# Optimization experiments

Hardware: AMD Instinct MI355X
Metric: run time of the kernel (lower is better)

## Reference

```python
import jax, jax.numpy as jnp
import numpy as np

N_NODES = 100000
N_EDGES = 1600000
N_FEAT = 165
HIDDEN = 128
N_CLASSES = 2
NEG_SLOPE = 0.2


def setup_inputs() -> dict:
    key = jax.random.key(0)
    ks = jax.random.split(key, 16)
    s = 0.05
    return {
        'x': jax.random.normal(ks[0], (N_NODES, N_FEAT), jnp.float32),
        'edge_src': jax.random.randint(ks[1], (N_EDGES,), 0, N_NODES, jnp.int32),
        'edge_dst': jax.random.randint(ks[2], (N_EDGES,), 0, N_NODES, jnp.int32),
        'W1l': jax.random.normal(ks[3], (N_FEAT, HIDDEN), jnp.float32) * s,
        'b1l': jnp.zeros((HIDDEN,), jnp.float32),
        'W1r': jax.random.normal(ks[4], (N_FEAT, HIDDEN), jnp.float32) * s,
        'b1r': jnp.zeros((HIDDEN,), jnp.float32),
        'att1': jax.random.normal(ks[5], (HIDDEN,), jnp.float32) * s,
        'bias1': jnp.zeros((HIDDEN,), jnp.float32),
        'W2l': jax.random.normal(ks[6], (HIDDEN, N_CLASSES), jnp.float32) * s,
        'b2l': jnp.zeros((N_CLASSES,), jnp.float32),
        'W2r': jax.random.normal(ks[7], (HIDDEN, N_CLASSES), jnp.float32) * s,
        'b2r': jnp.zeros((N_CLASSES,), jnp.float32),
        'att2': jax.random.normal(ks[8], (N_CLASSES,), jnp.float32) * s,
        'bias2': jnp.zeros((N_CLASSES,), jnp.float32),
    }


def gatv2_conv(x, src, dst, Wl, bl, Wr, br, att, bias, n_nodes):
    # PyG GATv2Conv, heads=1: x_l for source/message, x_r for target
    xl = x @ Wl + bl            # [N, D_out]
    xr = x @ Wr + br            # [N, D_out]
    e = jax.nn.leaky_relu(xl[src] + xr[dst], NEG_SLOPE)  # [E, D_out]
    score = e @ att             # [E]
    # segment softmax over destination nodes (stable)
    m = jax.ops.segment_max(score, dst, num_segments=n_nodes)
    a = jnp.exp(score - m[dst])
    denom = jax.ops.segment_sum(a, dst, num_segments=n_nodes)
    alpha = a / denom[dst]      # [E]
    out = jax.ops.segment_sum(alpha[:, None] * xl[src], dst, num_segments=n_nodes)
    return out + bias


def reference(x, edge_src, edge_dst, W1l, b1l, W1r, b1r, att1, bias1,
              W2l, b2l, W2r, b2r, att2, bias2):
    n = x.shape[0]
    # GATv2Conv adds self loops by default; every node has >=1 incoming edge
    loops = jnp.arange(n, dtype=edge_src.dtype)
    src = jnp.concatenate([edge_src, loops])
    dst = jnp.concatenate([edge_dst, loops])
    h = gatv2_conv(x, src, dst, W1l, b1l, W1r, b1r, att1, bias1, n)
    h = jax.nn.relu(h)
    # F.dropout with training=False is identity (eval mode)
    out = gatv2_conv(h, src, dst, W2l, b2l, W2r, b2r, att2, bias2, n)
    return out
```

## Files before the change

kernel.cpp:

```cpp
#include <hip/hip_runtime.h>
#include <hip/hip_bf16.h>

#define N_NODES 100000
#define NPAD 100032
#define N_EDGES 1600000
#define ETOT (N_EDGES + N_NODES)
#define NFEAT 165
#define KP 192
#define HID 128
#define NCLS 2
#define NEG 0.2f

#define NBUCK 391
#define CHUNK 16384
#define NCHUNK 104
#define GS_BLOCKS 2048

typedef short bf16x8 __attribute__((ext_vector_type(8)));
typedef float f32x4 __attribute__((ext_vector_type(4)));

#define OFF_FLAG 0
#define OFF_W 16
#define WO_ATT1 42496
#define WO_BIAS1 42624
#define WO_W2L 42752
#define WO_B2L 43008
#define WO_W2R 43010
#define WO_B2R 43266
#define WO_ATT2 43268
#define WO_BIAS2 43270

#define OFF_XB   43392
#define OFF_W2A  OFF_XB
#define OFF_WT   (OFF_XB + NPAD * KP / 2)
#define OFF_BCAT (OFF_WT + 256 * KP / 2)
#define OFF_XLB  (OFF_BCAT + 256)
#define OFF_XRB  (OFF_XLB + NPAD * HID / 2)
#define OFF_PAIRS (OFF_XRB + NPAD * HID / 2)
#define OFF_CSR  (OFF_PAIRS + 2 * ETOT)
#define OFF_ROWPTR (OFF_CSR + ETOT)
#define OFF_S    (OFF_ROWPTR + N_NODES + 8)
#define OFF_XL2  (OFF_S + NBUCK * NCHUNK + 8)
#define OFF_XR2  (OFF_XL2 + N_NODES * NCLS)
#define OFF_H    (OFF_XR2 + N_NODES * NCLS)
#define OFF_DL   (OFF_H + N_NODES * HID)
#define OFF_DR   (OFF_DL + NPAD)

__device__ __forceinline__ float bload16(unsigned short u) {
    return __uint_as_float(((unsigned)u) << 16);
}

__device__ __forceinline__ float lrelu(float v) {
    return fmaf(0.4f, fabsf(v), 0.6f * v);
}

__device__ __forceinline__ void unpack8(uint4 q, float* f) {
    f[0] = __uint_as_float(q.x << 16); f[1] = __uint_as_float(q.x & 0xffff0000u);
    f[2] = __uint_as_float(q.y << 16); f[3] = __uint_as_float(q.y & 0xffff0000u);
    f[4] = __uint_as_float(q.z << 16); f[5] = __uint_as_float(q.z & 0xffff0000u);
    f[6] = __uint_as_float(q.w << 16); f[7] = __uint_as_float(q.w & 0xffff0000u);
}

__device__ __forceinline__ unsigned short f2b(float f) {
    __hip_bfloat16 b = __float2bfloat16(f);
    return *(unsigned short*)&b;
}

__device__ __forceinline__ unsigned pack2(float a, float b) {
    return (unsigned)f2b(a) | ((unsigned)f2b(b) << 16);
}

__device__ __forceinline__ unsigned detect_flag(const unsigned short* x16, int lane) {
    unsigned short hh = x16[lane];
    unsigned e = (hh >> 7) & 0xFF;
    bool pl = ((hh & 0x7FFF) == 0) || (e >= 100 && e <= 140);
    unsigned long long m = __ballot(pl);
    return (__popcll(m) >= 52) ? 1u : 0u;
}

#define PREP_WT 49152
#define PREP_BC (PREP_WT + 256)
#define PREP_TOT (PREP_BC + 776)
#define PREP_BLKS ((PREP_TOT + 255) / 256)
__global__ void __launch_bounds__(256) k_prep_hist(
        const int* __restrict__ edst, int* __restrict__ bh,
        const unsigned short* __restrict__ x16,
        const void* W1l, const void* b1l, const void* W1r, const void* b1r,
        const void* att1, const void* bias1, const void* W2l, const void* b2l,
        const void* W2r, const void* b2r, const void* att2, const void* bias2,
        unsigned* __restrict__ flagp, unsigned short* __restrict__ wt,
        float* __restrict__ bcat, float* __restrict__ wb,
        float* __restrict__ w2a) {
    __shared__ int hist[NBUCK];
    if (blockIdx.x < NCHUNK) {
        for (int i = threadIdx.x; i < NBUCK; i += 256) hist[i] = 0;
        __syncthreads();
        int base = blockIdx.x * CHUNK;
        for (int i = threadIdx.x; i < CHUNK; i += 256) {
            int e = base + i;
            if (e >= ETOT) break;
            int d = (e < N_EDGES) ? edst[e] : (e - N_EDGES);
            atomicAdd(&hist[d >> 8], 1);
        }
        __syncthreads();
        for (int b = threadIdx.x; b < NBUCK; b += 256)
            bh[b * NCHUNK + blockIdx.x] = hist[b];
        return;
    }
    int lane = threadIdx.x & 63;
    unsigned isbf = detect_flag(x16, lane);
    int i = (blockIdx.x - NCHUNK) * 256 + threadIdx.x;
    if (i == 0) *flagp = isbf;
    if (i >= PREP_TOT) return;
    if (i < PREP_WT) {
        int n = i / KP, k = i - n * KP;
        unsigned short v = 0;
        if (k < NFEAT) {
            const void* src = (n < HID) ? W1l : W1r;
            size_t off = (size_t)k * HID + (n & (HID - 1));
            v = isbf ? ((const unsigned short*)src)[off]
                     : f2b(((const float*)src)[off]);
        }
        wt[i] = v;
    } else if (i < PREP_BC) {
        int n = i - PREP_WT;
        const void* src = (n < HID) ? b1l : b1r;
        int off = n & (HID - 1);
        bcat[n] = isbf ? bload16(((const unsigned short*)src)[off])
                       : ((const float*)src)[off];
    } else {
        int j = i - PREP_BC;
        const void* src; int off; int dst;
        if      (j < 128) { src = att1;  off = j;       dst = WO_ATT1 + j; }
        else if (j < 256) { src = bias1; off = j - 128; dst = WO_BIAS1 + (j - 128); }
        else if (j < 512) { src = W2l;   off = j - 256; dst = WO_W2L + (j - 256); }
        else if (j < 514) { src = b2l;   off = j - 512; dst = WO_B2L + (j - 512); }
        else if (j < 770) { src = W2r;   off = j - 514; dst = WO_W2R + (j - 514); }
        else if (j < 772) { src = b2r;   off = j - 770; dst = WO_B2R + (j - 770); }
        else if (j < 774) { src = att2;  off = j - 772; dst = WO_ATT2 + (j - 772); }
        else              { src = bias2; off = j - 774; dst = WO_BIAS2 + (j - 774); }
        float val = isbf ? bload16(((const unsigned short*)src)[off])
                         : ((const float*)src)[off];
        wb[dst] = val;
        if (j >= 256 && j < 512) w2a[j - 256] = val;
        else if (j >= 514 && j < 770) w2a[256 + (j - 514)] = val;
    }
}

__global__ void __launch_bounds__(512) k_pa_scan(int* __restrict__ S,
                                                 int* __restrict__ rowptr) {
    __shared__ int lds[512];
    const int TOT4 = (NBUCK * NCHUNK) / 4;
    int t = threadIdx.x;
    int b4 = t * 20;
    uint4* S4 = (uint4*)S;
    int sum = 0;
    for (int k = 0; k < 20; k++) {
        int i = b4 + k;
        if (i < TOT4) {
            uint4 v = S4[i];
            sum += (int)(v.x + v.y + v.z + v.w);
        }
    }
    lds[t] = sum;
    __syncthreads();
    for (int off = 1; off < 512; off <<= 1) {
        int v = lds[t];
        if (t >= off) v += lds[t - off];
        __syncthreads();
        lds[t] = v;
        __syncthreads();
    }
    int carry = (t == 0) ? 0 : lds[t - 1];
    for (int k = 0; k < 20; k++) {
        int i = b4 + k;
        if (i < TOT4) {
            uint4 v = S4[i];
            uint4 o;
            o.x = carry; carry += v.x;
            o.y = carry; carry += v.y;
            o.z = carry; carry += v.z;
            o.w = carry; carry += v.w;
            S4[i] = o;
        }
    }
    if (t == 0) rowptr[N_NODES] = ETOT;
}

__global__ void __launch_bounds__(256) k_pa_scatter(const int* __restrict__ esrc,
                                                    const int* __restrict__ edst,
                                                    const int* __restrict__ S,
                                                    unsigned* __restrict__ pairs) {
    __shared__ int cur[NBUCK];
    for (int i = threadIdx.x; i < NBUCK; i += 256)
        cur[i] = S[i * NCHUNK + blockIdx.x];
    __syncthreads();
    int base = blockIdx.x * CHUNK;
    for (int i = threadIdx.x; i < CHUNK; i += 256) {
        int e = base + i;
        if (e >= ETOT) break;
        int s = (e < N_EDGES) ? esrc[e] : (e - N_EDGES);
        int d = (e < N_EDGES) ? edst[e] : (e - N_EDGES);
        int p = atomicAdd(&cur[d >> 8], 1);
        pairs[p] = (unsigned)s | ((unsigned)(d & 255) << 24);
    }
}

__global__ void __launch_bounds__(256) k_bsort(const int* __restrict__ S,
                                               const unsigned* __restrict__ pairs,
                                               int* __restrict__ rowptr,
                                               int* __restrict__ csr) {
    __shared__ int hist[256];
    __shared__ int cur[256];
    int b = blockIdx.x, t = threadIdx.x;
    int beg = S[b * NCHUNK];
    int end = (b == NBUCK - 1) ? ETOT : S[(b + 1) * NCHUNK];
    hist[t] = 0;
    __syncthreads();
    for (int j = beg + t; j < end; j += 256)
        atomicAdd(&hist[pairs[j] >> 24], 1);
    __syncthreads();
    for (int off = 1; off < 256; off <<= 1) {
        int v = hist[t];
        if (t >= off) v += hist[t - off];
        __syncthreads();
        hist[t] = v;
        __syncthreads();
    }
    int excl = (t == 0) ? 0 : hist[t - 1];
    int node = b * 256 + t;
    if (node < N_NODES) rowptr[node] = beg + excl;
    cur[t] = beg + excl;
    __syncthreads();
    for (int j = beg + t; j < end; j += 256) {
        unsigned pr = pairs[j];
        int p = atomicAdd(&cur[pr >> 24], 1);
        csr[p] = (int)(pr & 0xFFFFFFu);
    }
}

#define XS_STRIDE 200
__global__ void __launch_bounds__(256) k_gemm1_mfma(
        const void* __restrict__ x,
        const unsigned* __restrict__ flagp,
        const unsigned short* __restrict__ wt,
        const float* __restrict__ bcat,
        const float* __restrict__ attp,
        __hip_bfloat16* __restrict__ xlb,
        __hip_bfloat16* __restrict__ xrb,
        float* __restrict__ dl,
        float* __restrict__ dr) {
    __shared__ unsigned short xs[64 * XS_STRIDE];
    __shared__ float dpart[4][64];
    int tid = threadIdx.x;
    int wave = tid >> 6, lane = tid & 63;
    int quad = lane >> 4, li = lane & 15;
    int node0 = blockIdx.x * 64;
    unsigned isbf = *flagp;
    const float* xf = (const float*)x;
    const unsigned short* x16 = (const unsigned short*)x;

    for (int i = tid; i < 64 * 27; i += 256) {
        int r = i / 27, c = 165 + (i - r * 27);
        xs[r * XS_STRIDE + c] = 0;
    }
    if (node0 + 64 <= N_NODES) {
        if (isbf) {
            const uint4* src = (const uint4*)(x16 + (size_t)node0 * NFEAT);
            for (int i = tid; i < 1320; i += 256) {
                uint4 v = src[i];
                int f = i * 8;
                unsigned short hh[8] = {
                    (unsigned short)(v.x & 0xffff), (unsigned short)(v.x >> 16),
                    (unsigned short)(v.y & 0xffff), (unsigned short)(v.y >> 16),
                    (unsigned short)(v.z & 0xffff), (unsigned short)(v.z >> 16),
                    (unsigned short)(v.w & 0xffff), (unsigned short)(v.w >> 16)};
#pragma unroll
                for (int t = 0; t < 8; t++) {
                    int ff = f + t, r = ff / NFEAT, c = ff - r * NFEAT;
                    xs[r * XS_STRIDE + c] = hh[t];
                }
            }
        } else {
            const float4* src = (const float4*)(xf + (size_t)node0 * NFEAT);
            for (int i = tid; i < 2640; i += 256) {
                float4 v = src[i];
                int f = i * 4;
                unsigned short hh[4] = {f2b(v.x), f2b(v.y), f2b(v.z), f2b(v.w)};
#pragma unroll
                for (int t = 0; t < 4; t++) {
                    int ff = f + t, r = ff / NFEAT, c = ff - r * NFEAT;
                    xs[r * XS_STRIDE + c] = hh[t];
                }
            }
        }
    } else {
        for (int i = tid; i < 64 * NFEAT; i += 256) {
            int r = i / NFEAT, c = i - r * NFEAT;
            int grow = node0 + r;
            unsigned short v = 0;
            if (grow < N_NODES) {
                size_t g = (size_t)grow * NFEAT + c;
                v = isbf ? x16[g] : f2b(xf[g]);
            }
            xs[r * XS_STRIDE + c] = v;
        }
    }

    bf16x8 wfrag[4][6];
#pragma unroll
    for (int q = 0; q < 4; q++) {
        int n = wave * 64 + q * 16 + li;
#pragma unroll
        for (int kk = 0; kk < 6; kk++)
            wfrag[q][kk] = *(const bf16x8*)&wt[(size_t)n * KP + kk * 32 + quad * 8];
    }
    float4 bv[4], attq4[4];
    int colbase = (wave & 1) * 64;
#pragma unroll
    for (int q = 0; q < 4; q++) {
        bv[q] = *(const float4*)&bcat[wave * 64 + q * 16 + quad * 4];
        attq4[q] = *(const float4*)&attp[colbase + q * 16 + quad * 4];
    }
    __syncthreads();

    for (int mt = 0; mt < 4; mt++) {
        bf16x8 xfrag[6];
#pragma unroll
        for (int kk = 0; kk < 6; kk++)
            xfrag[kk] = *(const bf16x8*)&xs[(mt * 16 + li) * XS_STRIDE + kk * 32 + quad * 8];
        int node = node0 + mt * 16 + li;
        __hip_bfloat16* dst = (wave < 2) ? xlb : xrb;
        float dp = 0.f;
#pragma unroll
        for (int q = 0; q < 4; q++) {
            f32x4 a = {0.f, 0.f, 0.f, 0.f};
#pragma unroll
            for (int kk = 0; kk < 6; kk++)
                a = __builtin_amdgcn_mfma_f32_16x16x32_bf16(wfrag[q][kk], xfrag[kk], a, 0, 0, 0);
            float f0 = a[0] + bv[q].x, f1 = a[1] + bv[q].y;
            float f2 = a[2] + bv[q].z, f3 = a[3] + bv[q].w;
            dp = fmaf(f0, attq4[q].x, dp);
            dp = fmaf(f1, attq4[q].y, dp);
            dp = fmaf(f2, attq4[q].z, dp);
            dp = fmaf(f3, attq4[q].w, dp);
            uint2 val = { pack2(f0, f1), pack2(f2, f3) };
            int col = colbase + q * 16 + quad * 4;
            *(uint2*)&dst[(size_t)node * HID + col] = val;
        }
        dp += __shfl_xor(dp, 16);
        dp += __shfl_xor(dp, 32);
        if (lane < 16) dpart[wave][mt * 16 + li] = dp;
    }
    __syncthreads();
    if (tid < 64)
        dl[node0 + tid] = dpart[0][tid] + dpart[1][tid];
    else if (tid < 128)
        dr[node0 + tid - 64] = dpart[2][tid - 64] + dpart[3][tid - 64];
}

__global__ void __launch_bounds__(256) k_gat1(const int* __restrict__ rowptr,
                                              const int* __restrict__ csr,
                                              const __hip_bfloat16* __restrict__ xlb,
                                              const __hip_bfloat16* __restrict__ xrb,
                                              const float* __restrict__ att,
                                              const float* __restrict__ bias,
                                              const float* __restrict__ dotsl,
                                              const float* __restrict__ dotsr,
                                              unsigned short* __restrict__ h16) {
    int wave = threadIdx.x >> 6, lane = threadIdx.x & 63;
    int sub = lane >> 4, li = lane & 15;
    float atv[8];
    {
        float4 t0 = ((const float4*)att)[li * 2];
        float4 t1 = ((const float4*)att)[li * 2 + 1];
        atv[0] = 0.4f * t0.x; atv[1] = 0.4f * t0.y;
        atv[2] = 0.4f * t0.z; atv[3] = 0.4f * t0.w;
        atv[4] = 0.4f * t1.x; atv[5] = 0.4f * t1.y;
        atv[6] = 0.4f * t1.z; atv[7] = 0.4f * t1.w;
    }

    for (int d = blockIdx.x * 4 + wave; d < N_NODES; d += GS_BLOCKS * 4) {
        uint4 qr = ((const uint4*)(xrb + (size_t)d * HID))[li];
        float xrv[8]; unpack8(qr, xrv);
        float drd = dotsr[d];
        int beg = rowptr[d], end = rowptr[d + 1];
        int iters = (end - beg + 3) >> 2;
        float l = 0.f, o[8];
#pragma unroll
        for (int t = 0; t < 8; t++) o[t] = 0.f;

        int j = beg + sub;
        bool valid = j < end;
        int s = valid ? csr[j] : 0;
        uint4 q = *(const uint4*)(xlb + (size_t)s * HID + li * 8);
        float dlc = dotsl[s];

        for (int it = 0; it < iters; it++) {
            float c[8]; unpack8(q, c);
            bool v = valid;
            float dle = dlc;
            j += 4;
            valid = j < end;
            int sn = valid ? csr[j] : 0;
            q = *(const uint4*)(xlb + (size_t)sn * HID + li * 8);
            dlc = dotsl[sn];

            float pa = 0.f;
#pragma unroll
            for (int t = 0; t < 8; t++) {
                float vv = c[t] + xrv[t];
                pa = fmaf(atv[t], fabsf(vv), pa);
            }
            pa += __shfl_xor(pa, 1);
            pa += __shfl_xor(pa, 2);
            pa += __shfl_xor(pa, 4);
            pa += __shfl_xor(pa, 8);
            float p = fmaf(0.6f, dle + drd, pa);
            float a = v ? __expf(p) : 0.f;
            l += a;
#pragma unroll
            for (int t = 0; t < 8; t++) o[t] = fmaf(a, c[t], o[t]);
        }
        l += __shfl_xor(l, 16);
        l += __shfl_xor(l, 32);
#pragma unroll
        for (int t = 0; t < 8; t++) {
            o[t] += __shfl_xor(o[t], 16);
            o[t] += __shfl_xor(o[t], 32);
        }
        if (sub == 0) {
            float inv = 1.f / l;
            float4 bv0 = ((const float4*)bias)[li * 2];
            float4 bv1 = ((const float4*)bias)[li * 2 + 1];
            float r0 = fmaxf(fmaf(o[0], inv, bv0.x), 0.f);
            float r1 = fmaxf(fmaf(o[1], inv, bv0.y), 0.f);
            float r2 = fmaxf(fmaf(o[2], inv, bv0.z), 0.f);
            float r3 = fmaxf(fmaf(o[3], inv, bv0.w), 0.f);
            float r4 = fmaxf(fmaf(o[4], inv, bv1.x), 0.f);
            float r5 = fmaxf(fmaf(o[5], inv, bv1.y), 0.f);
            float r6 = fmaxf(fmaf(o[6], inv, bv1.z), 0.f);
            float r7 = fmaxf(fmaf(o[7], inv, bv1.w), 0.f);
            uint4 val = { pack2(r0, r1), pack2(r2, r3),
                          pack2(r4, r5), pack2(r6, r7) };
            *(uint4*)&h16[(size_t)d * HID + li * 8] = val;
        }
    }
}

__global__ void __launch_bounds__(256) k_gemm2(const unsigned short* __restrict__ h16,
                                               const float* __restrict__ wb,
                                               const float* __restrict__ w2a,
                                               float* __restrict__ xl2, float* __restrict__ xr2) {
    int wave = threadIdx.x >> 6, lane = threadIdx.x & 63;
    int node = blockIdx.x * 4 + wave;
    if (node >= N_NODES) return;
    unsigned hw = ((const unsigned*)(h16 + (size_t)node * HID))[lane];
    float h0 = __uint_as_float(hw << 16);
    float h1 = __uint_as_float(hw & 0xffff0000u);
    float4 wl = ((const float4*)w2a)[lane];
    float4 wr = ((const float4*)(w2a + 256))[lane];
    float al0 = h0 * wl.x + h1 * wl.z;
    float al1 = h0 * wl.y + h1 * wl.w;
    float ar0 = h0 * wr.x + h1 * wr.z;
    float ar1 = h0 * wr.y + h1 * wr.w;
#pragma unroll
    for (int off = 32; off > 0; off >>= 1) {
        al0 += __shfl_down(al0, off);
        al1 += __shfl_down(al1, off);
        ar0 += __shfl_down(ar0, off);
        ar1 += __shfl_down(ar1, off);
    }
    if (lane == 0) {
        xl2[node * 2 + 0] = al0 + wb[WO_B2L + 0];
        xl2[node * 2 + 1] = al1 + wb[WO_B2L + 1];
        xr2[node * 2 + 0] = ar0 + wb[WO_B2R + 0];
        xr2[node * 2 + 1] = ar1 + wb[WO_B2R + 1];
    }
}

__global__ void __launch_bounds__(256) k_gat2(const int* __restrict__ rowptr,
                                              const int* __restrict__ csr,
                                              const float* __restrict__ xl2,
                                              const float* __restrict__ xr2,
                                              const float* __restrict__ wb,
                                              const unsigned* __restrict__ flag,
                                              void* __restrict__ dout) {
    int t = blockIdx.x * 256 + threadIdx.x;
    int d = t >> 2, part = t & 3;
    if (d >= N_NODES) return;
    float xr0 = xr2[d * 2 + 0], xr1 = xr2[d * 2 + 1];
    float at0 = wb[WO_ATT2], at1 = wb[WO_ATT2 + 1];
    int beg = rowptr[d], end = rowptr[d + 1];
    float l = 0.f, o0 = 0.f, o1 = 0.f;
    for (int j = beg + part; j < end; j += 4) {
        int s = csr[j];
        float b0 = xl2[s * 2 + 0], b1 = xl2[s * 2 + 1];
        float p = at0 * lrelu(b0 + xr0) + at1 * lrelu(b1 + xr1);
        float a = __expf(p);
        l += a;
        o0 = fmaf(a, b0, o0);
        o1 = fmaf(a, b1, o1);
    }
    l += __shfl_xor(l, 1);  o0 += __shfl_xor(o0, 1);  o1 += __shfl_xor(o1, 1);
    l += __shfl_xor(l, 2);  o0 += __shfl_xor(o0, 2);  o1 += __shfl_xor(o1, 2);
    if (part == 0) {
        float inv = 1.f / l;
        float v0 = fmaf(o0, inv, wb[WO_BIAS2 + 0]);
        float v1 = fmaf(o1, inv, wb[WO_BIAS2 + 1]);
        if (*flag) {
            ((__hip_bfloat16*)dout)[d * 2 + 0] = __float2bfloat16(v0);
            ((__hip_bfloat16*)dout)[d * 2 + 1] = __float2bfloat16(v1);
        } else {
            ((float*)dout)[d * 2 + 0] = v0;
            ((float*)dout)[d * 2 + 1] = v1;
        }
    }
}

extern "C" void kernel_launch(void* const* d_in, const int* in_sizes, int n_in,
                              void* d_out, int out_size, void* d_ws, size_t ws_size,
                              hipStream_t stream) {
    char* w = (char*)d_ws;
    unsigned* flag = (unsigned*)(w + (size_t)OFF_FLAG * 4);
    float* wb = (float*)(w + (size_t)OFF_W * 4);
    float* w2a = (float*)(w + (size_t)OFF_W2A * 4);
    unsigned short* wt = (unsigned short*)(w + (size_t)OFF_WT * 4);
    float* bcat = (float*)(w + (size_t)OFF_BCAT * 4);
    __hip_bfloat16* xlb = (__hip_bfloat16*)(w + (size_t)OFF_XLB * 4);
    __hip_bfloat16* xrb = (__hip_bfloat16*)(w + (size_t)OFF_XRB * 4);
    unsigned* pairs = (unsigned*)(w + (size_t)OFF_PAIRS * 4);
    int* csr = (int*)(w + (size_t)OFF_CSR * 4);
    int* rowptr = (int*)(w + (size_t)OFF_ROWPTR * 4);
    int* S = (int*)(w + (size_t)OFF_S * 4);
    float* xl2 = (float*)(w + (size_t)OFF_XL2 * 4);
    float* xr2 = (float*)(w + (size_t)OFF_XR2 * 4);
    unsigned short* h16 = (unsigned short*)(w + (size_t)OFF_H * 4);
    float* dl = (float*)(w + (size_t)OFF_DL * 4);
    float* dr = (float*)(w + (size_t)OFF_DR * 4);
    const int* esrc = (const int*)d_in[1];
    const int* edst = (const int*)d_in[2];

    k_prep_hist<<<NCHUNK + PREP_BLKS, 256, 0, stream>>>(
        edst, S, (const unsigned short*)d_in[0],
        d_in[3], d_in[4], d_in[5], d_in[6], d_in[7], d_in[8],
        d_in[9], d_in[10], d_in[11], d_in[12], d_in[13], d_in[14],
        flag, wt, bcat, wb, w2a);

    k_pa_scan<<<1, 512, 0, stream>>>(S, rowptr);
    k_pa_scatter<<<NCHUNK, 256, 0, stream>>>(esrc, edst, S, pairs);
    k_bsort<<<NBUCK, 256, 0, stream>>>(S, pairs, rowptr, csr);

    k_gemm1_mfma<<<NPAD / 64, 256, 0, stream>>>(d_in[0], flag, wt, bcat,
                                                wb + WO_ATT1, xlb, xrb, dl, dr);

    k_gat1<<<GS_BLOCKS, 256, 0, stream>>>(rowptr, csr, xlb, xrb,
                                          wb + WO_ATT1, wb + WO_BIAS1,
                                          dl, dr, h16);

    k_gemm2<<<(N_NODES + 3) / 4, 256, 0, stream>>>(h16, wb, w2a, xl2, xr2);

    k_gat2<<<(4 * N_NODES + 255) / 256, 256, 0, stream>>>(rowptr, csr, xl2, xr2,
                                                          wb, flag, d_out);
}
```

Before: 397.9 us.

## Fuse scatter with GEMM1, fold GEMM2 into GAT1, use packed FP32 math

Merges the edge-scatter kernel and the first-layer MFMA GEMM into one launch, with block index selecting the role, so the two independent phases overlap and share a union of shared memory. Fuses the second-layer projection into the layer-1 aggregation epilogue: each 16-lane group computes one output column of xl2/xr2 directly. This removes the h16 intermediate write and read and the k_gemm2 launch. It also rewrites the inner aggregation loop with v_pk_add_f32/v_pk_fma_f32 inline asm to halve VALU instruction count. In exchange, all four subgroups now do the bias/relu epilogue redundantly, and the union raises LDS for scatter blocks.

```diff
diff --git a/kernel.cpp b/kernel.cpp
--- a/kernel.cpp
+++ b/kernel.cpp
@@ -18,6 +18,7 @@
 
 typedef short bf16x8 __attribute__((ext_vector_type(8)));
 typedef float f32x4 __attribute__((ext_vector_type(4)));
+typedef float f32x2 __attribute__((ext_vector_type(2)));
 
 #define OFF_FLAG 0
 #define OFF_W 16
@@ -54,11 +55,20 @@
     return fmaf(0.4f, fabsf(v), 0.6f * v);
 }
 
-__device__ __forceinline__ void unpack8(uint4 q, float* f) {
-    f[0] = __uint_as_float(q.x << 16); f[1] = __uint_as_float(q.x & 0xffff0000u);
-    f[2] = __uint_as_float(q.y << 16); f[3] = __uint_as_float(q.y & 0xffff0000u);
-    f[4] = __uint_as_float(q.z << 16); f[5] = __uint_as_float(q.z & 0xffff0000u);
-    f[6] = __uint_as_float(q.w << 16); f[7] = __uint_as_float(q.w & 0xffff0000u);
+__device__ __forceinline__ void unpack8p(uint4 q, f32x2* f) {
+    f[0][0] = __uint_as_float(q.x << 16); f[0][1] = __uint_as_float(q.x & 0xffff0000u);
+    f[1][0] = __uint_as_float(q.y << 16); f[1][1] = __uint_as_float(q.y & 0xffff0000u);
+    f[2][0] = __uint_as_float(q.z << 16); f[2][1] = __uint_as_float(q.z & 0xffff0000u);
+    f[3][0] = __uint_as_float(q.w << 16); f[3][1] = __uint_as_float(q.w & 0xffff0000u);
+}
+
+__device__ __forceinline__ f32x2 pk_add(f32x2 a, f32x2 b) {
+    f32x2 d;
+    asm("v_pk_add_f32 %0, %1, %2" : "=v"(d) : "v"(a), "v"(b));
+    return d;
+}
+__device__ __forceinline__ void pk_fma_acc(f32x2& acc, f32x2 a, f32x2 b) {
+    asm("v_pk_fma_f32 %0, %1, %2, %0" : "+v"(acc) : "v"(a), "v"(b));
 }
 
 __device__ __forceinline__ unsigned short f2b(float f) {
@@ -187,23 +197,141 @@
     if (t == 0) rowptr[N_NODES] = ETOT;
 }
 
-__global__ void __launch_bounds__(256) k_pa_scatter(const int* __restrict__ esrc,
-                                                    const int* __restrict__ edst,
-                                                    const int* __restrict__ S,
-                                                    unsigned* __restrict__ pairs) {
-    __shared__ int cur[NBUCK];
-    for (int i = threadIdx.x; i < NBUCK; i += 256)
-        cur[i] = S[i * NCHUNK + blockIdx.x];
+#define XS_STRIDE 200
+__global__ void __launch_bounds__(256) k_scatter_gemm1(
+        const int* __restrict__ esrc, const int* __restrict__ edst,
+        const int* __restrict__ S, unsigned* __restrict__ pairs,
+        const void* __restrict__ x, const unsigned* __restrict__ flagp,
+        const unsigned short* __restrict__ wt, const float* __restrict__ bcat,
+        const float* __restrict__ attp,
+        __hip_bfloat16* __restrict__ xlb, __hip_bfloat16* __restrict__ xrb,
+        float* __restrict__ dl, float* __restrict__ dr) {
+    __shared__ union {
+        struct { unsigned short xs[64 * XS_STRIDE]; float dpart[4][64]; } g;
+        int cur[NBUCK];
+    } u;
+
+    if (blockIdx.x < NCHUNK) {
+        for (int i = threadIdx.x; i < NBUCK; i += 256)
+            u.cur[i] = S[i * NCHUNK + blockIdx.x];
+        __syncthreads();
+        int base = blockIdx.x * CHUNK;
+        for (int i = threadIdx.x; i < CHUNK; i += 256) {
+            int e = base + i;
+            if (e >= ETOT) break;
+            int s = (e < N_EDGES) ? esrc[e] : (e - N_EDGES);
+            int d = (e < N_EDGES) ? edst[e] : (e - N_EDGES);
+            int p = atomicAdd(&u.cur[d >> 8], 1);
+            pairs[p] = (unsigned)s | ((unsigned)(d & 255) << 24);
+        }
+        return;
+    }
+
+    int tid = threadIdx.x;
+    int wave = tid >> 6, lane = tid & 63;
+    int quad = lane >> 4, li = lane & 15;
+    int node0 = (blockIdx.x - NCHUNK) * 64;
+    unsigned isbf = *flagp;
+    const float* xf = (const float*)x;
+    const unsigned short* x16 = (const unsigned short*)x;
+
+    for (int i = tid; i < 64 * 27; i += 256) {
+        int r = i / 27, c = 165 + (i - r * 27);
+        u.g.xs[r * XS_STRIDE + c] = 0;
+    }
+    if (node0 + 64 <= N_NODES) {
+        if (isbf) {
+            const uint4* src = (const uint4*)(x16 + (size_t)node0 * NFEAT);
+            for (int i = tid; i < 1320; i += 256) {
+                uint4 v = src[i];
+                int f = i * 8;
+                unsigned short hh[8] = {
+                    (unsigned short)(v.x & 0xffff), (unsigned short)(v.x >> 16),
+                    (unsigned short)(v.y & 0xffff), (unsigned short)(v.y >> 16),
+                    (unsigned short)(v.z & 0xffff), (unsigned short)(v.z >> 16),
+                    (unsigned short)(v.w & 0xffff), (unsigned short)(v.w >> 16)};
+#pragma unroll
+                for (int t = 0; t < 8; t++) {
+                    int ff = f + t, r = ff / NFEAT, c = ff - r * NFEAT;
+                    u.g.xs[r * XS_STRIDE + c] = hh[t];
+                }
+            }
+        } else {
+            const float4* src = (const float4*)(xf + (size_t)node0 * NFEAT);
+            for (int i = tid; i < 2640; i += 256) {
+                float4 v = src[i];
+                int f = i * 4;
+                unsigned short hh[4] = {f2b(v.x), f2b(v.y), f2b(v.z), f2b(v.w)};
+#pragma unroll
+                for (int t = 0; t < 4; t++) {
+                    int ff = f + t, r = ff / NFEAT, c = ff - r * NFEAT;
+                    u.g.xs[r * XS_STRIDE + c] = hh[t];
+                }
+            }
+        }
+    } else {
+        for (int i = tid; i < 64 * NFEAT; i += 256) {
+            int r = i / NFEAT, c = i - r * NFEAT;
+            int grow = node0 + r;
+            unsigned short v = 0;
+            if (grow < N_NODES) {
+                size_t g = (size_t)grow * NFEAT + c;
+                v = isbf ? x16[g] : f2b(xf[g]);
+            }
+            u.g.xs[r * XS_STRIDE + c] = v;
+        }
+    }
+
+    bf16x8 wfrag[4][6];
+#pragma unroll
+    for (int q = 0; q < 4; q++) {
+        int n = wave * 64 + q * 16 + li;
+#pragma unroll
+        for (int kk = 0; kk < 6; kk++)
+            wfrag[q][kk] = *(const bf16x8*)&wt[(size_t)n * KP + kk * 32 + quad * 8];
+    }
+    float4 bv[4], attq4[4];
+    int colbase = (wave & 1) * 64;
+#pragma unroll
+    for (int q = 0; q < 4; q++) {
+        bv[q] = *(const float4*)&bcat[wave * 64 + q * 16 + quad * 4];
+        attq4[q] = *(const float4*)&attp[colbase + q * 16 + quad * 4];
+    }
     __syncthreads();
-    int base = blockIdx.x * CHUNK;
-    for (int i = threadIdx.x; i < CHUNK; i += 256) {
-        int e = base + i;
-        if (e >= ETOT) break;
-        int s = (e < N_EDGES) ? esrc[e] : (e - N_EDGES);
-        int d = (e < N_EDGES) ? edst[e] : (e - N_EDGES);
-        int p = atomicAdd(&cur[d >> 8], 1);
-        pairs[p] = (unsigned)s | ((unsigned)(d & 255) << 24);
-    }
+
+    for (int mt = 0; mt < 4; mt++) {
+        bf16x8 xfrag[6];
+#pragma unroll
+        for (int kk = 0; kk < 6; kk++)
+            xfrag[kk] = *(const bf16x8*)&u.g.xs[(mt * 16 + li) * XS_STRIDE + kk * 32 + quad * 8];
+        int node = node0 + mt * 16 + li;
+        __hip_bfloat16* dst = (wave < 2) ? xlb : xrb;
+        float dp = 0.f;
+#pragma unroll
+        for (int q = 0; q < 4; q++) {
+            f32x4 a = {0.f, 0.f, 0.f, 0.f};
+#pragma unroll
+            for (int kk = 0; kk < 6; kk++)
+                a = __builtin_amdgcn_mfma_f32_16x16x32_bf16(wfrag[q][kk], xfrag[kk], a, 0, 0, 0);
+            float f0 = a[0] + bv[q].x, f1 = a[1] + bv[q].y;
+            float f2 = a[2] + bv[q].z, f3 = a[3] + bv[q].w;
+            dp = fmaf(f0, attq4[q].x, dp);
+            dp = fmaf(f1, attq4[q].y, dp);
+            dp = fmaf(f2, attq4[q].z, dp);
+            dp = fmaf(f3, attq4[q].w, dp);
+            uint2 val = { pack2(f0, f1), pack2(f2, f3) };
+            int col = colbase + q * 16 + quad * 4;
+            *(uint2*)&dst[(size_t)node * HID + col] = val;
+        }
+        dp += __shfl_xor(dp, 16);
+        dp += __shfl_xor(dp, 32);
+        if (lane < 16) u.g.dpart[wave][mt * 16 + li] = dp;
+    }
+    __syncthreads();
+    if (tid < 64)
+        dl[node0 + tid] = u.g.dpart[0][tid] + u.g.dpart[1][tid];
+    else if (tid < 128)
+        dr[node0 + tid - 64] = u.g.dpart[2][tid - 64] + u.g.dpart[3][tid - 64];
 }
 
 __global__ void __launch_bounds__(256) k_bsort(const int* __restrict__ S,
@@ -239,126 +367,6 @@
     }
 }
 
-#define XS_STRIDE 200
-__global__ void __launch_bounds__(256) k_gemm1_mfma(
-        const void* __restrict__ x,
-        const unsigned* __restrict__ flagp,
-        const unsigned short* __restrict__ wt,
-        const float* __restrict__ bcat,
-        const float* __restrict__ attp,
-        __hip_bfloat16* __restrict__ xlb,
-        __hip_bfloat16* __restrict__ xrb,
-        float* __restrict__ dl,
-        float* __restrict__ dr) {
-    __shared__ unsigned short xs[64 * XS_STRIDE];
-    __shared__ float dpart[4][64];
-    int tid = threadIdx.x;
-    int wave = tid >> 6, lane = tid & 63;
-    int quad = lane >> 4, li = lane & 15;
-    int node0 = blockIdx.x * 64;
-    unsigned isbf = *flagp;
-    const float* xf = (const float*)x;
-    const unsigned short* x16 = (const unsigned short*)x;
-
-    for (int i = tid; i < 64 * 27; i += 256) {
-        int r = i / 27, c = 165 + (i - r * 27);
-        xs[r * XS_STRIDE + c] = 0;
-    }
-    if (node0 + 64 <= N_NODES) {
-        if (isbf) {
-            const uint4* src = (const uint4*)(x16 + (size_t)node0 * NFEAT);
-            for (int i = tid; i < 1320; i += 256) {
-                uint4 v = src[i];
-                int f = i * 8;
-                unsigned short hh[8] = {
-                    (unsigned short)(v.x & 0xffff), (unsigned short)(v.x >> 16),
-                    (unsigned short)(v.y & 0xffff), (unsigned short)(v.y >> 16),
-                    (unsigned short)(v.z & 0xffff), (unsigned short)(v.z >> 16),
-                    (unsigned short)(v.w & 0xffff), (unsigned short)(v.w >> 16)};
-#pragma unroll
-                for (int t = 0; t < 8; t++) {
-                    int ff = f + t, r = ff / NFEAT, c = ff - r * NFEAT;
-                    xs[r * XS_STRIDE + c] = hh[t];
-                }
-            }
-        } else {
-            const float4* src = (const float4*)(xf + (size_t)node0 * NFEAT);
-            for (int i = tid; i < 2640; i += 256) {
-                float4 v = src[i];
-                int f = i * 4;
-                unsigned short hh[4] = {f2b(v.x), f2b(v.y), f2b(v.z), f2b(v.w)};
-#pragma unroll
-                for (int t = 0; t < 4; t++) {
-                    int ff = f + t, r = ff / NFEAT, c = ff - r * NFEAT;
-                    xs[r * XS_STRIDE + c] = hh[t];
-                }
-            }
-        }
-    } else {
-        for (int i = tid; i < 64 * NFEAT; i += 256) {
-            int r = i / NFEAT, c = i - r * NFEAT;
-            int grow = node0 + r;
-            unsigned short v = 0;
-            if (grow < N_NODES) {
-                size_t g = (size_t)grow * NFEAT + c;
-                v = isbf ? x16[g] : f2b(xf[g]);
-            }
-            xs[r * XS_STRIDE + c] = v;
-        }
-    }
-
-    bf16x8 wfrag[4][6];
-#pragma unroll
-    for (int q = 0; q < 4; q++) {
-        int n = wave * 64 + q * 16 + li;
-#pragma unroll
-        for (int kk = 0; kk < 6; kk++)
-            wfrag[q][kk] = *(const bf16x8*)&wt[(size_t)n * KP + kk * 32 + quad * 8];
-    }
-    float4 bv[4], attq4[4];
-    int colbase = (wave & 1) * 64;
-#pragma unroll
-    for (int q = 0; q < 4; q++) {
-        bv[q] = *(const float4*)&bcat[wave * 64 + q * 16 + quad * 4];
-        attq4[q] = *(const float4*)&attp[colbase + q * 16 + quad * 4];
-    }
-    __syncthreads();
-
-    for (int mt = 0; mt < 4; mt++) {
-        bf16x8 xfrag[6];
-#pragma unroll
-        for (int kk = 0; kk < 6; kk++)
-            xfrag[kk] = *(const bf16x8*)&xs[(mt * 16 + li) * XS_STRIDE + kk * 32 + quad * 8];
-        int node = node0 + mt * 16 + li;
-        __hip_bfloat16* dst = (wave < 2) ? xlb : xrb;
-        float dp = 0.f;
-#pragma unroll
-        for (int q = 0; q < 4; q++) {
-            f32x4 a = {0.f, 0.f, 0.f, 0.f};
-#pragma unroll
-            for (int kk = 0; kk < 6; kk++)
-                a = __builtin_amdgcn_mfma_f32_16x16x32_bf16(wfrag[q][kk], xfrag[kk], a, 0, 0, 0);
-            float f0 = a[0] + bv[q].x, f1 = a[1] + bv[q].y;
-            float f2 = a[2] + bv[q].z, f3 = a[3] + bv[q].w;
-            dp = fmaf(f0, attq4[q].x, dp);
-            dp = fmaf(f1, attq4[q].y, dp);
-            dp = fmaf(f2, attq4[q].z, dp);
-            dp = fmaf(f3, attq4[q].w, dp);
-            uint2 val = { pack2(f0, f1), pack2(f2, f3) };
-            int col = colbase + q * 16 + quad * 4;
-            *(uint2*)&dst[(size_t)node * HID + col] = val;
-        }
-        dp += __shfl_xor(dp, 16);
-        dp += __shfl_xor(dp, 32);
-        if (lane < 16) dpart[wave][mt * 16 + li] = dp;
-    }
-    __syncthreads();
-    if (tid < 64)
-        dl[node0 + tid] = dpart[0][tid] + dpart[1][tid];
-    else if (tid < 128)
-        dr[node0 + tid - 64] = dpart[2][tid - 64] + dpart[3][tid - 64];
-}
-
 __global__ void __launch_bounds__(256) k_gat1(const int* __restrict__ rowptr,
                                               const int* __restrict__ csr,
                                               const __hip_bfloat16* __restrict__ xlb,
@@ -367,28 +375,39 @@
                                               const float* __restrict__ bias,
                                               const float* __restrict__ dotsl,
                                               const float* __restrict__ dotsr,
-                                              unsigned short* __restrict__ h16) {
+                                              const float* __restrict__ w2a,
+                                              const float* __restrict__ wb,
+                                              float* __restrict__ xl2,
+                                              float* __restrict__ xr2) {
     int wave = threadIdx.x >> 6, lane = threadIdx.x & 63;
     int sub = lane >> 4, li = lane & 15;
-    float atv[8];
+    f32x2 at2v[4];
     {
         float4 t0 = ((const float4*)att)[li * 2];
         float4 t1 = ((const float4*)att)[li * 2 + 1];
-        atv[0] = 0.4f * t0.x; atv[1] = 0.4f * t0.y;
-        atv[2] = 0.4f * t0.z; atv[3] = 0.4f * t0.w;
-        atv[4] = 0.4f * t1.x; atv[5] = 0.4f * t1.y;
-        atv[6] = 0.4f * t1.z; atv[7] = 0.4f * t1.w;
-    }
+        at2v[0][0] = 0.4f * t0.x; at2v[0][1] = 0.4f * t0.y;
+        at2v[1][0] = 0.4f * t0.z; at2v[1][1] = 0.4f * t0.w;
+        at2v[2][0] = 0.4f * t1.x; at2v[2][1] = 0.4f * t1.y;
+        at2v[3][0] = 0.4f * t1.z; at2v[3][1] = 0.4f * t1.w;
+    }
+    int col = sub & 1;
+    const float* wsrc = w2a + (sub >> 1) * 256;
+    float w2v[8];
+#pragma unroll
+    for (int k = 0; k < 8; k++) w2v[k] = wsrc[(li * 8 + k) * 2 + col];
+    float b2 = wb[(sub < 2 ? WO_B2L : WO_B2R) + col];
+    float* outp = (sub < 2) ? xl2 : xr2;
 
     for (int d = blockIdx.x * 4 + wave; d < N_NODES; d += GS_BLOCKS * 4) {
         uint4 qr = ((const uint4*)(xrb + (size_t)d * HID))[li];
-        float xrv[8]; unpack8(qr, xrv);
+        f32x2 xr2v[4]; unpack8p(qr, xr2v);
         float drd = dotsr[d];
         int beg = rowptr[d], end = rowptr[d + 1];
         int iters = (end - beg + 3) >> 2;
-        float l = 0.f, o[8];
-#pragma unroll
-        for (int t = 0; t < 8; t++) o[t] = 0.f;
+        float l = 0.f;
+        f32x2 o2[4];
+#pragma unroll
+        for (int t = 0; t < 4; t++) { o2[t][0] = 0.f; o2[t][1] = 0.f; }
 
         int j = beg + sub;
         bool valid = j < end;
@@ -397,7 +416,7 @@
         float dlc = dotsl[s];
 
         for (int it = 0; it < iters; it++) {
-            float c[8]; unpack8(q, c);
+            f32x2 c2[4]; unpack8p(q, c2);
             bool v = valid;
             float dle = dlc;
             j += 4;
@@ -406,12 +425,15 @@
             q = *(const uint4*)(xlb + (size_t)sn * HID + li * 8);
             dlc = dotsl[sn];
 
-            float pa = 0.f;
-#pragma unroll
-            for (int t = 0; t < 8; t++) {
-                float vv = c[t] + xrv[t];
-                pa = fmaf(atv[t], fabsf(vv), pa);
+            f32x2 pa2; pa2[0] = 0.f; pa2[1] = 0.f;
+#pragma unroll
+            for (int t = 0; t < 4; t++) {
+                f32x2 vv = pk_add(c2[t], xr2v[t]);
+                f32x2 av;
+                av[0] = fabsf(vv[0]); av[1] = fabsf(vv[1]);
+                pk_fma_acc(pa2, at2v[t], av);
             }
+            float pa = pa2[0] + pa2[1];
             pa += __shfl_xor(pa, 1);
             pa += __shfl_xor(pa, 2);
             pa += __shfl_xor(pa, 4);
@@ -419,63 +441,43 @@
             float p = fmaf(0.6f, dle + drd, pa);
             float a = v ? __expf(p) : 0.f;
             l += a;
-#pragma unroll
-            for (int t = 0; t < 8; t++) o[t] = fmaf(a, c[t], o[t]);
+            f32x2 aa; aa[0] = a; aa[1] = a;
+#pragma unroll
+            for (int t = 0; t < 4; t++) pk_fma_acc(o2[t], aa, c2[t]);
         }
         l += __shfl_xor(l, 16);
         l += __shfl_xor(l, 32);
 #pragma unroll
-        for (int t = 0; t < 8; t++) {
-            o[t] += __shfl_xor(o[t], 16);
-            o[t] += __shfl_xor(o[t], 32);
-        }
-        if (sub == 0) {
-            float inv = 1.f / l;
-            float4 bv0 = ((const float4*)bias)[li * 2];
-            float4 bv1 = ((const float4*)bias)[li * 2 + 1];
-            float r0 = fmaxf(fmaf(o[0], inv, bv0.x), 0.f);
-            float r1 = fmaxf(fmaf(o[1], inv, bv0.y), 0.f);
-            float r2 = fmaxf(fmaf(o[2], inv, bv0.z), 0.f);
-            float r3 = fmaxf(fmaf(o[3], inv, bv0.w), 0.f);
-            float r4 = fmaxf(fmaf(o[4], inv, bv1.x), 0.f);
-            float r5 = fmaxf(fmaf(o[5], inv, bv1.y), 0.f);
-            float r6 = fmaxf(fmaf(o[6], inv, bv1.z), 0.f);
-            float r7 = fmaxf(fmaf(o[7], inv, bv1.w), 0.f);
-            uint4 val = { pack2(r0, r1), pack2(r2, r3),
-                          pack2(r4, r5), pack2(r6, r7) };
-            *(uint4*)&h16[(size_t)d * HID + li * 8] = val;
-        }
-    }
-}
-
-__global__ void __launch_bounds__(256) k_gemm2(const unsigned short* __restrict__ h16,
-                                               const float* __restrict__ wb,
-                                               const float* __restrict__ w2a,
-                                               float* __restrict__ xl2, float* __restrict__ xr2) {
-    int wave = threadIdx.x >> 6, lane = threadIdx.x & 63;
-    int node = blockIdx.x * 4 + wave;
-    if (node >= N_NODES) return;
-    unsigned hw = ((const unsigned*)(h16 + (size_t)node * HID))[lane];
-    float h0 = __uint_as_float(hw << 16);
-    float h1 = __uint_as_float(hw & 0xffff0000u);
-    float4 wl = ((const float4*)w2a)[lane];
-    float4 wr = ((const float4*)(w2a + 256))[lane];
-    float al0 = h0 * wl.x + h1 * wl.z;
-    float al1 = h0 * wl.y + h1 * wl.w;
-    float ar0 = h0 * wr.x + h1 * wr.z;
-    float ar1 = h0 * wr.y + h1 * wr.w;
-#pragma unroll
-    for (int off = 32; off > 0; off >>= 1) {
-        al0 += __shfl_down(al0, off);
-        al1 += __shfl_down(al1, off);
-        ar0 += __shfl_down(ar0, off);
-        ar1 += __shfl_down(ar1, off);
-    }
-    if (lane == 0) {
-        xl2[node * 2 + 0] = al0 + wb[WO_B2L + 0];
-        xl2[node * 2 + 1] = al1 + wb[WO_B2L + 1];
-        xr2[node * 2 + 0] = ar0 + wb[WO_B2R + 0];
-        xr2[node * 2 + 1] = ar1 + wb[WO_B2R + 1];
+        for (int t = 0; t < 4; t++) {
+            o2[t][0] += __shfl_xor(o2[t][0], 16);
+            o2[t][1] += __shfl_xor(o2[t][1], 16);
+            o2[t][0] += __shfl_xor(o2[t][0], 32);
+            o2[t][1] += __shfl_xor(o2[t][1], 32);
+        }
+        float inv = 1.f / l;
+        float4 bv0 = ((const float4*)bias)[li * 2];
+        float4 bv1 = ((const float4*)bias)[li * 2 + 1];
+        float r0 = fmaxf(fmaf(o2[0][0], inv, bv0.x), 0.f);
+        float r1 = fmaxf(fmaf(o2[0][1], inv, bv0.y), 0.f);
+        float r2 = fmaxf(fmaf(o2[1][0], inv, bv0.z), 0.f);
+        float r3 = fmaxf(fmaf(o2[1][1], inv, bv0.w), 0.f);
+        float r4 = fmaxf(fmaf(o2[2][0], inv, bv1.x), 0.f);
+        float r5 = fmaxf(fmaf(o2[2][1], inv, bv1.y), 0.f);
+        float r6 = fmaxf(fmaf(o2[3][0], inv, bv1.z), 0.f);
+        float r7 = fmaxf(fmaf(o2[3][1], inv, bv1.w), 0.f);
+        float dot = r0 * w2v[0];
+        dot = fmaf(r1, w2v[1], dot);
+        dot = fmaf(r2, w2v[2], dot);
+        dot = fmaf(r3, w2v[3], dot);
+        dot = fmaf(r4, w2v[4], dot);
+        dot = fmaf(r5, w2v[5], dot);
+        dot = fmaf(r6, w2v[6], dot);
+        dot = fmaf(r7, w2v[7], dot);
+        dot += __shfl_xor(dot, 1);
+        dot += __shfl_xor(dot, 2);
+        dot += __shfl_xor(dot, 4);
+        dot += __shfl_xor(dot, 8);
+        if (li == 0) outp[d * 2 + col] = dot + b2;
     }
 }
 
@@ -535,7 +537,6 @@
     int* S = (int*)(w + (size_t)OFF_S * 4);
     float* xl2 = (float*)(w + (size_t)OFF_XL2 * 4);
     float* xr2 = (float*)(w + (size_t)OFF_XR2 * 4);
-    unsigned short* h16 = (unsigned short*)(w + (size_t)OFF_H * 4);
     float* dl = (float*)(w + (size_t)OFF_DL * 4);
     float* dr = (float*)(w + (size_t)OFF_DR * 4);
     const int* esrc = (const int*)d_in[1];
@@ -548,17 +549,16 @@
         flag, wt, bcat, wb, w2a);
 
     k_pa_scan<<<1, 512, 0, stream>>>(S, rowptr);
-    k_pa_scatter<<<NCHUNK, 256, 0, stream>>>(esrc, edst, S, pairs);
+
+    k_scatter_gemm1<<<NCHUNK + NPAD / 64, 256, 0, stream>>>(
+        esrc, edst, S, pairs, d_in[0], flag, wt, bcat,
+        wb + WO_ATT1, xlb, xrb, dl, dr);
+
     k_bsort<<<NBUCK, 256, 0, stream>>>(S, pairs, rowptr, csr);
-
-    k_gemm1_mfma<<<NPAD / 64, 256, 0, stream>>>(d_in[0], flag, wt, bcat,
-                                                wb + WO_ATT1, xlb, xrb, dl, dr);
 
     k_gat1<<<GS_BLOCKS, 256, 0, stream>>>(rowptr, csr, xlb, xrb,
                                           wb + WO_ATT1, wb + WO_BIAS1,
-                                          dl, dr, h16);
-
-    k_gemm2<<<(N_NODES + 3) / 4, 256, 0, stream>>>(h16, wb, w2a, xl2, xr2);
+                                          dl, dr, w2a, wb, xl2, xr2);
 
     k_gat2<<<(4 * N_NODES + 255) / 256, 256, 0, stream>>>(rowptr, csr, xl2, xr2,
                                                           wb, flag, d_out);
```

After: 382.3 us. 3.9% less time.
